# Performance work log

Hardware: AMD Instinct MI355X
Metric: run time of the kernel (lower is better)

## Reference

```python
import jax, jax.numpy as jnp
import numpy as np

NUM_HEADS = 16
D_MODEL = 1024
NUM_LAYERS = 4
VOCAB = 32000
SEQ_LEN = 1024
BATCH = 4
EPS = 1e-6


def position_embedding(seq_len, d_model):
    pos = jnp.arange(seq_len, dtype=jnp.float32)[:, None]
    i = jnp.arange(d_model, dtype=jnp.float32)[None, :]
    # faithful to source: angle_rates = 1 / (1/10000)^(2*(i//2)/d) = 10000^(2*(i//2)/d)
    angle_rates = jnp.power(10000.0, 2.0 * jnp.floor(i / 2.0) / float(d_model))
    ang = pos * angle_rates  # [S, D]
    return jnp.concatenate([jnp.sin(ang[:, 0::2]), jnp.cos(ang[:, 1::2])], axis=-1)[None]  # [1,S,D]


def layer_norm(x, g, b):
    m = jnp.mean(x, axis=-1, keepdims=True)
    v = jnp.mean(jnp.square(x - m), axis=-1, keepdims=True)
    return (x - m) * jax.lax.rsqrt(v + EPS) * g + b


def setup_inputs() -> dict:
    key = jax.random.key(0)
    ks = jax.random.split(key, 20)
    L, D = NUM_LAYERS, D_MODEL
    s = 0.02
    inp = {
        "x": jax.random.randint(ks[0], (BATCH, SEQ_LEN), 0, VOCAB, dtype=jnp.int32),
        "mask": jnp.zeros((BATCH, 1, 1, SEQ_LEN), dtype=jnp.float32),
        "emb": jax.random.normal(ks[1], (VOCAB, D), dtype=jnp.float32) * s,
        "wq": jax.random.normal(ks[2], (L, D, D), dtype=jnp.float32) * s,
        "bq": jnp.zeros((L, D), dtype=jnp.float32),
        "wk": jax.random.normal(ks[3], (L, D, D), dtype=jnp.float32) * s,
        "bk": jnp.zeros((L, D), dtype=jnp.float32),
        "wv": jax.random.normal(ks[4], (L, D, D), dtype=jnp.float32) * s,
        "bv": jnp.zeros((L, D), dtype=jnp.float32),
        "wo": jax.random.normal(ks[5], (L, D, D), dtype=jnp.float32) * s,
        "bo": jnp.zeros((L, D), dtype=jnp.float32),
        "wf": jax.random.normal(ks[6], (L, D, D), dtype=jnp.float32) * s,
        "bf": jnp.zeros((L, D), dtype=jnp.float32),
        "g1": jnp.ones((L, D), dtype=jnp.float32),
        "b1": jnp.zeros((L, D), dtype=jnp.float32),
        "g2": jnp.ones((L, D), dtype=jnp.float32),
        "b2": jnp.zeros((L, D), dtype=jnp.float32),
    }
    return inp


def encoder_forward(x, mask, emb, wq, bq, wk, bk, wv, bv, wo, bo, wf, bf, g1, b1, g2, b2):
    B, S = x.shape
    D = emb.shape[1]
    H = NUM_HEADS
    dh = D // H
    h = emb[x] * jnp.sqrt(jnp.float32(D))  # [B,S,D]
    h = h + position_embedding(S, D)[:, :S, :]

    def split_heads(t):  # [B,S,D] -> [B,H,S,dh]
        return t.reshape(B, S, H, dh).transpose(0, 2, 1, 3)

    for l in range(wq.shape[0]):
        q = split_heads(h @ wq[l] + bq[l])
        k = split_heads(h @ wk[l] + bk[l])
        v = split_heads(h @ wv[l] + bv[l])
        scores = jnp.einsum("bhqd,bhkd->bhqk", q, k) / jnp.sqrt(jnp.float32(dh))
        scores = scores + mask * -1e9
        w = jax.nn.softmax(scores, axis=-1)
        ctx = jnp.einsum("bhqk,bhkd->bhqd", w, v)  # [B,H,S,dh]
        ctx = ctx.transpose(0, 2, 1, 3).reshape(B, S, D)
        attn_out = ctx @ wo[l] + bo[l]
        h = layer_norm(h + attn_out, g1[l], b1[l])
        ff = h @ wf[l] + bf[l]
        h = layer_norm(h + ff, g2[l], b2[l])
    return h


def reference(x, mask, emb, wq, bq, wk, bk, wv, bv, wo, bo, wf, bf, g1, b1, g2, b2):
    return encoder_forward(x, mask, emb, wq, bq, wk, bk, wv, bv, wo, bo, wf, bf, g1, b1, g2, b2)
```

## Files before the change

### kernel.cpp

```cpp
#include <hip/hip_runtime.h>
#include <hip/hip_bf16.h>
#include <math.h>

typedef __hip_bfloat16 bf16;
typedef unsigned int u32;
typedef __attribute__((ext_vector_type(8))) short short8;
typedef __attribute__((ext_vector_type(4))) float f32x4;


#define ATT_LDK 72
#define PS_LD  72

typedef __attribute__((address_space(3))) u32 lds_u32;
typedef const __attribute__((address_space(1))) u32 glb_u32;
static __device__ __forceinline__ void g2l16(const void* g, void* l) {
    __builtin_amdgcn_global_load_lds((glb_u32*)g, (lds_u32*)l, 16, 0, 0);
}

static __device__ __forceinline__ unsigned short bf16bits(float f) {
    bf16 h = __float2bfloat16(f);
    return *(unsigned short*)&h;
}

__global__ __launch_bounds__(256) void wprep_kernel(
    const float* __restrict__ wq, const float* __restrict__ wk,
    const float* __restrict__ wv, const float* __restrict__ wo,
    const float* __restrict__ wf, bf16* __restrict__ wt_all)
{
    __shared__ bf16 tile[64][ATT_LDK];
    const int z = blockIdx.z;
    const int l = z / 5, f = z % 5;
    const float* src = (f == 0) ? wq : (f == 1) ? wk : (f == 2) ? wv : (f == 3) ? wo : wf;
    src += (size_t)l * 1024 * 1024;
    bf16* dst = wt_all + ((size_t)l * 5 + f) * 1024 * 1024;

    const int k0 = blockIdx.x * 64, n0 = blockIdx.y * 64;
    const int t = threadIdx.x;
#pragma unroll
    for (int rr = 0; rr < 4; ++rr) {
        int slot = t + rr * 256;
        int r = slot >> 4, c = slot & 15;
        float4 v = *(const float4*)(src + (size_t)(k0 + r) * 1024 + n0 + c * 4);
        tile[c * 4 + 0][r] = __float2bfloat16(v.x);
        tile[c * 4 + 1][r] = __float2bfloat16(v.y);
        tile[c * 4 + 2][r] = __float2bfloat16(v.z);
        tile[c * 4 + 3][r] = __float2bfloat16(v.w);
    }
    __syncthreads();
#pragma unroll
    for (int rr = 0; rr < 2; ++rr) {
        int slot = t + rr * 256;
        int n = slot >> 3, c = slot & 7;
        *(uint4*)(dst + (size_t)(n0 + n) * 1024 + k0 + c * 8) = *(const uint4*)&tile[n][c * 8];
    }
}

__global__ void bias_stack_kernel(const float* __restrict__ bq, const float* __restrict__ bk,
                                  const float* __restrict__ bv, float* __restrict__ bqkv)
{
    int i = blockIdx.x * 256 + threadIdx.x;
    if (i < 4 * 3072) {
        int l = i / 3072, c = i % 3072;
        int fam = c >> 10, cc = c & 1023;
        const float* s = (fam == 0) ? bq : (fam == 1) ? bk : bv;
        bqkv[i] = s[l * 1024 + cc];
    }
}

__global__ __launch_bounds__(256) void pe_kernel(float* __restrict__ pe)
{
    int idx = blockIdx.x * 256 + threadIdx.x;
    int d0 = (idx & 255) * 4;
    int s = idx >> 8;
    float out[4];
#pragma unroll
    for (int j = 0; j < 4; ++j) {
        int d = d0 + j;
        int m = (d < 512) ? d : (d - 512);
        float ex = (float)(2 * m) * (1.0f / 1024.0f);
        float rate = (float)pow(10000.0, (double)ex);
        float ang = (float)s * rate;
        double a = (double)ang;
        out[j] = (d < 512) ? (float)sin(a) : (float)cos(a);
    }
    *(float4*)(pe + (size_t)s * 1024 + d0) = *(float4*)out;
}

__global__ __launch_bounds__(256) void embed_kernel(
    const int* __restrict__ x, const float* __restrict__ emb,
    const float* __restrict__ pe,
    float* __restrict__ hf, bf16* __restrict__ hb)
{
    int idx = blockIdx.x * 256 + threadIdx.x;
    int d0 = (idx & 255) * 4;
    int row = idx >> 8;
    int s = row & 1023;
    int tok = x[row];
    float4 e = *(const float4*)(emb + (size_t)tok * 1024 + d0);
    float4 p = *(const float4*)(pe + (size_t)s * 1024 + d0);
    float out[4] = {e.x * 32.0f + p.x, e.y * 32.0f + p.y,
                    e.z * 32.0f + p.z, e.w * 32.0f + p.w};
    *(float4*)(hf + (size_t)row * 1024 + d0) = *(float4*)out;
    unsigned short pk[4];
#pragma unroll
    for (int j = 0; j < 4; ++j) pk[j] = bf16bits(out[j]);
    *(uint2*)(hb + (size_t)row * 1024 + d0) = *(uint2*)pk;
}

__global__ __launch_bounds__(256, 3) void gemm_bt_kernel(
    const bf16* __restrict__ A, const bf16* __restrict__ Bt,
    const float* __restrict__ bias,
    bf16* __restrict__ Cb, bf16* __restrict__ VtOut,
    int M, int N, int K)
{
    __shared__ bf16 As[128 * 32];
    __shared__ bf16 Bs[128 * 32];
    __shared__ bf16 Cst[4][16 * PS_LD];
    const int t = threadIdx.x;
    const int lane = t & 63, wave = t >> 6;
    const int wr = wave >> 1, wc = wave & 1;
    const int lidx = lane & 15, quad = lane >> 4;
    const int m0 = blockIdx.x * 128, n0 = blockIdx.y * 128;

    f32x4 acc[4][4];
#pragma unroll
    for (int i = 0; i < 4; ++i)
#pragma unroll
        for (int j = 0; j < 4; ++j) acc[i][j] = (f32x4){0.f, 0.f, 0.f, 0.f};

    const int r0 = wave * 32;
    const int rloc = lane >> 2;
    const int csw = ((lane & 3) ^ ((lane >> 3) & 3)) * 8;
    const bf16* Abase = A  + (size_t)(m0 + r0 + rloc) * K + csw;
    const bf16* Bbase = Bt + (size_t)(n0 + r0 + rloc) * K + csw;
    bf16* AsW = As + r0 * 32;
    bf16* BsW = Bs + r0 * 32;
    const int aslot = (quad ^ ((lidx >> 1) & 3)) * 8;

    for (int k0 = 0; k0 < K; k0 += 32) {
        __syncthreads();
        g2l16(Abase + k0,                  AsW);
        g2l16(Abase + k0 + 16 * (size_t)K, AsW + 16 * 32);
        g2l16(Bbase + k0,                  BsW);
        g2l16(Bbase + k0 + 16 * (size_t)K, BsW + 16 * 32);
        __syncthreads();

        short8 af[4], bfr[4];
#pragma unroll
        for (int i = 0; i < 4; ++i)
            af[i] = *(const short8*)(As + (wr * 64 + i * 16 + lidx) * 32 + aslot);
#pragma unroll
        for (int j = 0; j < 4; ++j)
            bfr[j] = *(const short8*)(Bs + (wc * 64 + j * 16 + lidx) * 32 + aslot);
#pragma unroll
        for (int i = 0; i < 4; ++i)
#pragma unroll
            for (int j = 0; j < 4; ++j)
                acc[i][j] = __builtin_amdgcn_mfma_f32_16x16x32_bf16(af[i], bfr[j], acc[i][j], 0, 0, 0);
    }

    float bvj[4];
#pragma unroll
    for (int j = 0; j < 4; ++j)
        bvj[j] = bias ? bias[n0 + wc * 64 + j * 16 + lidx] : 0.0f;

    if (VtOut && n0 >= 2048) {
        const int bidx = m0 >> 10;
        const int s_base = (m0 & 1023) + wr * 64 + quad * 4;
        const int d_base = (n0 - 2048) + wc * 64;
#pragma unroll
        for (int i = 0; i < 4; ++i)
#pragma unroll
            for (int j = 0; j < 4; ++j) {
                unsigned short pk[4];
#pragma unroll
                for (int r = 0; r < 4; ++r)
                    pk[r] = bf16bits(acc[i][j][r] + bvj[j]);
                bf16* dst = VtOut + ((size_t)bidx * 1024 + d_base + j * 16 + lidx) * 1024
                            + s_base + i * 16;
                *(uint2*)dst = *(const uint2*)pk;
            }
    } else {
        const int row16 = lane >> 2, c4 = lane & 3;
#pragma unroll
        for (int i = 0; i < 4; ++i) {
#pragma unroll
            for (int j = 0; j < 4; ++j)
#pragma unroll
                for (int r = 0; r < 4; ++r)
                    Cst[wave][(quad * 4 + r) * PS_LD + j * 16 + lidx] =
                        __float2bfloat16(acc[i][j][r] + bvj[j]);
            bf16* dst = Cb + (size_t)(m0 + wr * 64 + i * 16 + row16) * N + n0 + wc * 64;
            const bf16* srcr = &Cst[wave][row16 * PS_LD];
#pragma unroll
            for (int h = 0; h < 2; ++h)
                *(uint4*)(dst + (c4 + 4 * h) * 8) = *(const uint4*)(srcr + (c4 + 4 * h) * 8);
        }
    }
}

__global__ __launch_bounds__(256, 4) void gemm64_kernel(
    const bf16* __restrict__ A, const bf16* __restrict__ Bt,
    const float* __restrict__ bias, float* __restrict__ Cf,
    int M, int N, int K)
{
    __shared__ bf16 As[64 * 32];
    __shared__ bf16 Bs[128 * 32];
    const int t = threadIdx.x;
    const int lane = t & 63, wave = t >> 6;
    const int wr = wave >> 1, wc = wave & 1;
    const int lidx = lane & 15, quad = lane >> 4;
    const int m0 = blockIdx.x * 64, n0 = blockIdx.y * 128;

    f32x4 acc[2][4];
#pragma unroll
    for (int i = 0; i < 2; ++i)
#pragma unroll
        for (int j = 0; j < 4; ++j) acc[i][j] = (f32x4){0.f, 0.f, 0.f, 0.f};

    const int rloc = lane >> 2;
    const int csw = ((lane & 3) ^ ((lane >> 3) & 3)) * 8;
    const bf16* Abase = A  + (size_t)(m0 + wave * 16 + rloc) * K + csw;
    const bf16* Bbase = Bt + (size_t)(n0 + wave * 32 + rloc) * K + csw;
    bf16* AsW = As + wave * 16 * 32;
    bf16* BsW = Bs + wave * 32 * 32;
    const int aslot = (quad ^ ((lidx >> 1) & 3)) * 8;

    for (int k0 = 0; k0 < K; k0 += 32) {
        __syncthreads();
        g2l16(Abase + k0,                  AsW);
        g2l16(Bbase + k0,                  BsW);
        g2l16(Bbase + k0 + 16 * (size_t)K, BsW + 16 * 32);
        __syncthreads();

        short8 af[2], bfr[4];
#pragma unroll
        for (int i = 0; i < 2; ++i)
            af[i] = *(const short8*)(As + (wr * 32 + i * 16 + lidx) * 32 + aslot);
#pragma unroll
        for (int j = 0; j < 4; ++j)
            bfr[j] = *(const short8*)(Bs + (wc * 64 + j * 16 + lidx) * 32 + aslot);
#pragma unroll
        for (int i = 0; i < 2; ++i)
#pragma unroll
            for (int j = 0; j < 4; ++j)
                acc[i][j] = __builtin_amdgcn_mfma_f32_16x16x32_bf16(af[i], bfr[j], acc[i][j], 0, 0, 0);
    }

#pragma unroll
    for (int i = 0; i < 2; ++i)
#pragma unroll
        for (int j = 0; j < 4; ++j) {
            int col = n0 + wc * 64 + j * 16 + lidx;
            float bv = bias[col];
#pragma unroll
            for (int r = 0; r < 4; ++r) {
                int rowg = m0 + wr * 32 + i * 16 + quad * 4 + r;
                Cf[(size_t)rowg * N + col] = acc[i][j][r] + bv;
            }
        }
}

__global__ __launch_bounds__(512, 4) void attention_kernel(
    const bf16* __restrict__ QKV,
    const bf16* __restrict__ Vt,
    const float* __restrict__ mask,
    bf16* __restrict__ ctx)
{
    __shared__ bf16 Ks[64 * 64];
    __shared__ bf16 Vs[64 * 64];
    __shared__ bf16 Ps[8][16 * PS_LD];

    const int t = threadIdx.x, lane = t & 63, wave = t >> 6;
    const int quad = lane >> 4, lidx = lane & 15;
    const int b = blockIdx.x >> 4, hh = blockIdx.x & 15;
    const int q0 = blockIdx.y * 128 + wave * 16;

    const int r8 = lane >> 3;
    const int gc = ((lane & 7) ^ r8) * 8;
    const bf16* kg0 = QKV + (size_t)(b * 1024 + wave * 8 + r8) * 3072 + 1024 + hh * 64 + gc;
    const bf16* vg0 = Vt  + (size_t)(b * 1024 + hh * 64 + wave * 8 + r8) * 1024 + gc;
    bf16* KsW = Ks + wave * 8 * 64;
    bf16* VsW = Vs + wave * 8 * 64;

    short8 qf[2];
    {
        const bf16* qp = QKV + (size_t)(b * 1024 + q0 + lidx) * 3072 + hh * 64;
        qf[0] = *(const short8*)(qp + quad * 8);
        qf[1] = *(const short8*)(qp + 32 + quad * 8);
    }

    f32x4 Oacc[4];
#pragma unroll
    for (int nt = 0; nt < 4; ++nt) Oacc[nt] = (f32x4){0.f, 0.f, 0.f, 0.f};
    float psum[4] = {0.f, 0.f, 0.f, 0.f};

    const int fslot = lidx & 7;

    for (int kt = 0; kt < 16; ++kt) {
        __syncthreads();
        g2l16(kg0 + (size_t)kt * 64 * 3072, KsW);
        g2l16(vg0 + kt * 64, VsW);
        __syncthreads();

        f32x4 sacc[4];
#pragma unroll
        for (int nt = 0; nt < 4; ++nt) sacc[nt] = (f32x4){0.f, 0.f, 0.f, 0.f};
#pragma unroll
        for (int kk = 0; kk < 2; ++kk)
#pragma unroll
            for (int nt = 0; nt < 4; ++nt) {
                short8 kf = *(const short8*)(Ks + (nt * 16 + lidx) * 64 + (((kk * 4 + quad) ^ fslot) * 8));
                sacc[nt] = __builtin_amdgcn_mfma_f32_16x16x32_bf16(qf[kk], kf, sacc[nt], 0, 0, 0);
            }

#pragma unroll
        for (int nt = 0; nt < 4; ++nt) {
            float mv = mask[b * 1024 + kt * 64 + nt * 16 + lidx] * -1e9f;
#pragma unroll
            for (int r = 0; r < 4; ++r) {
                float p = __expf(sacc[nt][r] * 0.125f + mv);
                sacc[nt][r] = p;
                psum[r] += p;
            }
        }

#pragma unroll
        for (int nt = 0; nt < 4; ++nt)
#pragma unroll
            for (int r = 0; r < 4; ++r)
                Ps[wave][(quad * 4 + r) * PS_LD + nt * 16 + lidx] = __float2bfloat16(sacc[nt][r]);

#pragma unroll
        for (int kk = 0; kk < 2; ++kk) {
            short8 pf = *(const short8*)(&Ps[wave][lidx * PS_LD + kk * 32 + quad * 8]);
#pragma unroll
            for (int nt = 0; nt < 4; ++nt) {
                short8 vf = *(const short8*)(Vs + (nt * 16 + lidx) * 64 + (((kk * 4 + quad) ^ fslot) * 8));
                Oacc[nt] = __builtin_amdgcn_mfma_f32_16x16x32_bf16(pf, vf, Oacc[nt], 0, 0, 0);
            }
        }
    }

#pragma unroll
    for (int off = 1; off < 16; off <<= 1)
#pragma unroll
        for (int r = 0; r < 4; ++r)
            psum[r] += __shfl_xor(psum[r], off, 64);
    float linv[4];
#pragma unroll
    for (int r = 0; r < 4; ++r) linv[r] = 1.0f / psum[r];

#pragma unroll
    for (int nt = 0; nt < 4; ++nt)
#pragma unroll
        for (int r = 0; r < 4; ++r)
            Ps[wave][(quad * 4 + r) * PS_LD + nt * 16 + lidx] = __float2bfloat16(Oacc[nt][r] * linv[r]);

    const int row16 = lane >> 2, c4 = lane & 3;
    bf16* dst = ctx + (size_t)(b * 1024 + q0 + row16) * 1024 + hh * 64;
    const bf16* srcr = &Ps[wave][row16 * PS_LD];
#pragma unroll
    for (int h = 0; h < 2; ++h)
        *(uint4*)(dst + (c4 + 4 * h) * 8) = *(const uint4*)(srcr + (c4 + 4 * h) * 8);
}

__global__ __launch_bounds__(256) void add_ln_kernel(
    const float* __restrict__ x, const float* __restrict__ dx,
    const float* __restrict__ g, const float* __restrict__ b,
    float* __restrict__ outf, bf16* __restrict__ outb)
{
    __shared__ float red[4];
    const int row = blockIdx.x;
    const int t = threadIdx.x;
    const int c0 = t * 4;
    float4 xv = *(const float4*)(x + (size_t)row * 1024 + c0);
    float4 dv = *(const float4*)(dx + (size_t)row * 1024 + c0);
    float v[4] = {xv.x + dv.x, xv.y + dv.y, xv.z + dv.z, xv.w + dv.w};
    float s = v[0] + v[1] + v[2] + v[3];
#pragma unroll
    for (int off = 1; off < 64; off <<= 1) s += __shfl_xor(s, off, 64);
    if ((t & 63) == 0) red[t >> 6] = s;
    __syncthreads();
    float mean = (red[0] + red[1] + red[2] + red[3]) * (1.0f / 1024.0f);
    float sq = 0.f;
#pragma unroll
    for (int i = 0; i < 4; ++i) { float d = v[i] - mean; sq += d * d; }
#pragma unroll
    for (int off = 1; off < 64; off <<= 1) sq += __shfl_xor(sq, off, 64);
    __syncthreads();
    if ((t & 63) == 0) red[t >> 6] = sq;
    __syncthreads();
    float var = (red[0] + red[1] + red[2] + red[3]) * (1.0f / 1024.0f);
    float rs = rsqrtf(var + 1e-6f);
    float4 gv = *(const float4*)(g + c0);
    float4 bv = *(const float4*)(b + c0);
    float gg[4] = {gv.x, gv.y, gv.z, gv.w}, bb[4] = {bv.x, bv.y, bv.z, bv.w};
    float o[4];
    unsigned short pk[4];
#pragma unroll
    for (int i = 0; i < 4; ++i) {
        o[i] = (v[i] - mean) * rs * gg[i] + bb[i];
        pk[i] = bf16bits(o[i]);
    }
    *(float4*)(outf + (size_t)row * 1024 + c0) = *(float4*)o;
    *(uint2*)(outb + (size_t)row * 1024 + c0) = *(uint2*)pk;
}

extern "C" void kernel_launch(void* const* d_in, const int* in_sizes, int n_in,
                              void* d_out, int out_size, void* d_ws, size_t ws_size,
                              hipStream_t stream)
{
    const int*   x    = (const int*)d_in[0];
    const float* mask = (const float*)d_in[1];
    const float* emb  = (const float*)d_in[2];
    const float* wq   = (const float*)d_in[3];
    const float* bq   = (const float*)d_in[4];
    const float* wk   = (const float*)d_in[5];
    const float* bk   = (const float*)d_in[6];
    const float* wv   = (const float*)d_in[7];
    const float* bv   = (const float*)d_in[8];
    const float* wo   = (const float*)d_in[9];
    const float* bo   = (const float*)d_in[10];
    const float* wf   = (const float*)d_in[11];
    const float* bfp  = (const float*)d_in[12];
    const float* g1   = (const float*)d_in[13];
    const float* b1   = (const float*)d_in[14];
    const float* g2   = (const float*)d_in[15];
    const float* b2   = (const float*)d_in[16];

    char* ws = (char*)d_ws;
    float* h_f  = (float*)ws;                 ws += 4096ull * 1024 * 4;
    bf16*  h_b  = (bf16*)ws;                  ws += 4096ull * 1024 * 2;
    bf16*  qkv  = (bf16*)ws;                  ws += 4096ull * 3072 * 2;
    bf16*  vt   = (bf16*)ws;                  ws += 4096ull * 1024 * 2;
    bf16*  ctx  = (bf16*)ws;                  ws += 4096ull * 1024 * 2;
    bf16*  wt   = (bf16*)ws;                  ws += 20ull * 1024 * 1024 * 2;
    float* pe   = (float*)ws;                 ws += 1024ull * 1024 * 4;
    float* bqkv = (float*)ws;                 ws += 4ull * 3072 * 4;
    float* delta = (float*)qkv;

    wprep_kernel<<<dim3(16, 16, 20), 256, 0, stream>>>(wq, wk, wv, wo, wf, wt);
    bias_stack_kernel<<<dim3(48), 256, 0, stream>>>(bq, bk, bv, bqkv);
    pe_kernel<<<dim3(1024), 256, 0, stream>>>(pe);
    embed_kernel<<<dim3(4096), 256, 0, stream>>>(x, emb, pe, h_f, h_b);

    for (int l = 0; l < 4; ++l) {
        bf16* wt_l = wt + (size_t)l * 5 * 1024 * 1024;
        gemm_bt_kernel<<<dim3(32, 24), 256, 0, stream>>>(
            h_b, wt_l, bqkv + l * 3072, qkv, vt, 4096, 3072, 1024);
        attention_kernel<<<dim3(64, 8), 512, 0, stream>>>(qkv, vt, mask, ctx);
        gemm64_kernel<<<dim3(64, 8), 256, 0, stream>>>(
            ctx, wt_l + 3ull * 1024 * 1024, bo + l * 1024, delta, 4096, 1024, 1024);
        add_ln_kernel<<<dim3(4096), 256, 0, stream>>>(
            h_f, delta, g1 + l * 1024, b1 + l * 1024, h_f, h_b);
        gemm64_kernel<<<dim3(64, 8), 256, 0, stream>>>(
            h_b, wt_l + 4ull * 1024 * 1024, bfp + l * 1024, delta, 4096, 1024, 1024);
        float* outf = (l == 3) ? (float*)d_out : h_f;
        add_ln_kernel<<<dim3(4096), 256, 0, stream>>>(
            h_f, delta, g2 + l * 1024, b2 + l * 1024, outf, h_b);
    }
    (void)in_sizes; (void)n_in; (void)out_size; (void)ws_size;
}
```

Before: 782.2 us.

## Split-K 128x128 GEMM for out/FF projections and smaller attention blocks

Replaces the 64x128 output/FFN GEMM with a 128x128 tile kernel that splits K in two, writing two fp32 partial buffers that the add+LayerNorm kernel sums. This raises per-block data reuse while keeping the block count at 512. Attention is also changed from 512-thread blocks covering 128 queries to 256-thread blocks covering 64 queries, doubling the grid, with each wave loading twice as many K/V rows. The trade-off is an extra 16MB fp32 partial write and read per GEMM, plus more redundant K/V loading in attention.

```diff
diff --git a/kernel.cpp b/kernel.cpp
--- a/kernel.cpp
+++ b/kernel.cpp
@@ -199,69 +199,74 @@
     }
 }
 
-__global__ __launch_bounds__(256, 4) void gemm64_kernel(
+__global__ __launch_bounds__(256, 2) void gemm_sk_kernel(
     const bf16* __restrict__ A, const bf16* __restrict__ Bt,
     const float* __restrict__ bias, float* __restrict__ Cf,
     int M, int N, int K)
 {
-    __shared__ bf16 As[64 * 32];
+    __shared__ bf16 As[128 * 32];
     __shared__ bf16 Bs[128 * 32];
     const int t = threadIdx.x;
     const int lane = t & 63, wave = t >> 6;
     const int wr = wave >> 1, wc = wave & 1;
     const int lidx = lane & 15, quad = lane >> 4;
-    const int m0 = blockIdx.x * 64, n0 = blockIdx.y * 128;
-
-    f32x4 acc[2][4];
-#pragma unroll
-    for (int i = 0; i < 2; ++i)
+    const int m0 = blockIdx.x * 128, n0 = blockIdx.y * 128;
+    const int kz = blockIdx.z;
+    const int kbeg = kz * (K >> 1), kend = kbeg + (K >> 1);
+
+    f32x4 acc[4][4];
+#pragma unroll
+    for (int i = 0; i < 4; ++i)
 #pragma unroll
         for (int j = 0; j < 4; ++j) acc[i][j] = (f32x4){0.f, 0.f, 0.f, 0.f};
 
+    const int r0 = wave * 32;
     const int rloc = lane >> 2;
     const int csw = ((lane & 3) ^ ((lane >> 3) & 3)) * 8;
-    const bf16* Abase = A  + (size_t)(m0 + wave * 16 + rloc) * K + csw;
-    const bf16* Bbase = Bt + (size_t)(n0 + wave * 32 + rloc) * K + csw;
-    bf16* AsW = As + wave * 16 * 32;
-    bf16* BsW = Bs + wave * 32 * 32;
+    const bf16* Abase = A  + (size_t)(m0 + r0 + rloc) * K + csw;
+    const bf16* Bbase = Bt + (size_t)(n0 + r0 + rloc) * K + csw;
+    bf16* AsW = As + r0 * 32;
+    bf16* BsW = Bs + r0 * 32;
     const int aslot = (quad ^ ((lidx >> 1) & 3)) * 8;
 
-    for (int k0 = 0; k0 < K; k0 += 32) {
+    for (int k0 = kbeg; k0 < kend; k0 += 32) {
         __syncthreads();
         g2l16(Abase + k0,                  AsW);
+        g2l16(Abase + k0 + 16 * (size_t)K, AsW + 16 * 32);
         g2l16(Bbase + k0,                  BsW);
         g2l16(Bbase + k0 + 16 * (size_t)K, BsW + 16 * 32);
         __syncthreads();
 
-        short8 af[2], bfr[4];
-#pragma unroll
-        for (int i = 0; i < 2; ++i)
-            af[i] = *(const short8*)(As + (wr * 32 + i * 16 + lidx) * 32 + aslot);
+        short8 af[4], bfr[4];
+#pragma unroll
+        for (int i = 0; i < 4; ++i)
+            af[i] = *(const short8*)(As + (wr * 64 + i * 16 + lidx) * 32 + aslot);
 #pragma unroll
         for (int j = 0; j < 4; ++j)
             bfr[j] = *(const short8*)(Bs + (wc * 64 + j * 16 + lidx) * 32 + aslot);
 #pragma unroll
-        for (int i = 0; i < 2; ++i)
+        for (int i = 0; i < 4; ++i)
 #pragma unroll
             for (int j = 0; j < 4; ++j)
                 acc[i][j] = __builtin_amdgcn_mfma_f32_16x16x32_bf16(af[i], bfr[j], acc[i][j], 0, 0, 0);
     }
 
-#pragma unroll
-    for (int i = 0; i < 2; ++i)
+    float* out = Cf + (size_t)kz * M * N;
+#pragma unroll
+    for (int i = 0; i < 4; ++i)
 #pragma unroll
         for (int j = 0; j < 4; ++j) {
             int col = n0 + wc * 64 + j * 16 + lidx;
-            float bv = bias[col];
+            float bv = (kz == 0) ? bias[col] : 0.0f;
 #pragma unroll
             for (int r = 0; r < 4; ++r) {
-                int rowg = m0 + wr * 32 + i * 16 + quad * 4 + r;
-                Cf[(size_t)rowg * N + col] = acc[i][j][r] + bv;
+                int rowg = m0 + wr * 64 + i * 16 + quad * 4 + r;
+                out[(size_t)rowg * N + col] = acc[i][j][r] + bv;
             }
         }
 }
 
-__global__ __launch_bounds__(512, 4) void attention_kernel(
+__global__ __launch_bounds__(256, 4) void attention_kernel(
     const bf16* __restrict__ QKV,
     const bf16* __restrict__ Vt,
     const float* __restrict__ mask,
@@ -269,19 +274,19 @@
 {
     __shared__ bf16 Ks[64 * 64];
     __shared__ bf16 Vs[64 * 64];
-    __shared__ bf16 Ps[8][16 * PS_LD];
+    __shared__ bf16 Ps[4][16 * PS_LD];
 
     const int t = threadIdx.x, lane = t & 63, wave = t >> 6;
     const int quad = lane >> 4, lidx = lane & 15;
     const int b = blockIdx.x >> 4, hh = blockIdx.x & 15;
-    const int q0 = blockIdx.y * 128 + wave * 16;
+    const int q0 = blockIdx.y * 64 + wave * 16;
 
     const int r8 = lane >> 3;
     const int gc = ((lane & 7) ^ r8) * 8;
-    const bf16* kg0 = QKV + (size_t)(b * 1024 + wave * 8 + r8) * 3072 + 1024 + hh * 64 + gc;
-    const bf16* vg0 = Vt  + (size_t)(b * 1024 + hh * 64 + wave * 8 + r8) * 1024 + gc;
-    bf16* KsW = Ks + wave * 8 * 64;
-    bf16* VsW = Vs + wave * 8 * 64;
+    const bf16* kg0 = QKV + (size_t)(b * 1024 + wave * 16 + r8) * 3072 + 1024 + hh * 64 + gc;
+    const bf16* vg0 = Vt  + (size_t)(b * 1024 + hh * 64 + wave * 16 + r8) * 1024 + gc;
+    bf16* KsW = Ks + wave * 16 * 64;
+    bf16* VsW = Vs + wave * 16 * 64;
 
     short8 qf[2];
     {
@@ -299,8 +304,10 @@
 
     for (int kt = 0; kt < 16; ++kt) {
         __syncthreads();
-        g2l16(kg0 + (size_t)kt * 64 * 3072, KsW);
-        g2l16(vg0 + kt * 64, VsW);
+        g2l16(kg0 + (size_t)kt * 64 * 3072,       KsW);
+        g2l16(kg0 + (size_t)(kt * 64 + 8) * 3072, KsW + 8 * 64);
+        g2l16(vg0 + kt * 64,                      VsW);
+        g2l16(vg0 + 8 * 1024 + kt * 64,           VsW + 8 * 64);
         __syncthreads();
 
         f32x4 sacc[4];
@@ -366,7 +373,8 @@
 }
 
 __global__ __launch_bounds__(256) void add_ln_kernel(
-    const float* __restrict__ x, const float* __restrict__ dx,
+    const float* __restrict__ x, const float* __restrict__ dx0,
+    const float* __restrict__ dx1,
     const float* __restrict__ g, const float* __restrict__ b,
     float* __restrict__ outf, bf16* __restrict__ outb)
 {
@@ -375,8 +383,10 @@
     const int t = threadIdx.x;
     const int c0 = t * 4;
     float4 xv = *(const float4*)(x + (size_t)row * 1024 + c0);
-    float4 dv = *(const float4*)(dx + (size_t)row * 1024 + c0);
-    float v[4] = {xv.x + dv.x, xv.y + dv.y, xv.z + dv.z, xv.w + dv.w};
+    float4 d0 = *(const float4*)(dx0 + (size_t)row * 1024 + c0);
+    float4 d1 = *(const float4*)(dx1 + (size_t)row * 1024 + c0);
+    float v[4] = {xv.x + d0.x + d1.x, xv.y + d0.y + d1.y,
+                  xv.z + d0.z + d1.z, xv.w + d0.w + d1.w};
     float s = v[0] + v[1] + v[2] + v[3];
 #pragma unroll
     for (int off = 1; off < 64; off <<= 1) s += __shfl_xor(s, off, 64);
@@ -430,15 +440,16 @@
     const float* b2   = (const float*)d_in[16];
 
     char* ws = (char*)d_ws;
-    float* h_f  = (float*)ws;                 ws += 4096ull * 1024 * 4;
-    bf16*  h_b  = (bf16*)ws;                  ws += 4096ull * 1024 * 2;
-    bf16*  qkv  = (bf16*)ws;                  ws += 4096ull * 3072 * 2;
-    bf16*  vt   = (bf16*)ws;                  ws += 4096ull * 1024 * 2;
-    bf16*  ctx  = (bf16*)ws;                  ws += 4096ull * 1024 * 2;
-    bf16*  wt   = (bf16*)ws;                  ws += 20ull * 1024 * 1024 * 2;
-    float* pe   = (float*)ws;                 ws += 1024ull * 1024 * 4;
-    float* bqkv = (float*)ws;                 ws += 4ull * 3072 * 4;
-    float* delta = (float*)qkv;
+    float* h_f   = (float*)ws;                ws += 4096ull * 1024 * 4;
+    bf16*  h_b   = (bf16*)ws;                 ws += 4096ull * 1024 * 2;
+    bf16*  qkv   = (bf16*)ws;                 ws += 4096ull * 3072 * 2;
+    bf16*  vt    = (bf16*)ws;                 ws += 4096ull * 1024 * 2;
+    bf16*  ctx   = (bf16*)ws;                 ws += 4096ull * 1024 * 2;
+    bf16*  wt    = (bf16*)ws;                 ws += 20ull * 1024 * 1024 * 2;
+    float* pe    = (float*)ws;                ws += 1024ull * 1024 * 4;
+    float* delta = (float*)ws;                ws += 2ull * 4096 * 1024 * 4;
+    float* bqkv  = (float*)ws;                ws += 4ull * 3072 * 4;
+    float* delta1 = delta + 4096ull * 1024;
 
     wprep_kernel<<<dim3(16, 16, 20), 256, 0, stream>>>(wq, wk, wv, wo, wf, wt);
     bias_stack_kernel<<<dim3(48), 256, 0, stream>>>(bq, bk, bv, bqkv);
@@ -449,16 +460,16 @@
         bf16* wt_l = wt + (size_t)l * 5 * 1024 * 1024;
         gemm_bt_kernel<<<dim3(32, 24), 256, 0, stream>>>(
             h_b, wt_l, bqkv + l * 3072, qkv, vt, 4096, 3072, 1024);
-        attention_kernel<<<dim3(64, 8), 512, 0, stream>>>(qkv, vt, mask, ctx);
-        gemm64_kernel<<<dim3(64, 8), 256, 0, stream>>>(
+        attention_kernel<<<dim3(64, 16), 256, 0, stream>>>(qkv, vt, mask, ctx);
+        gemm_sk_kernel<<<dim3(32, 8, 2), 256, 0, stream>>>(
             ctx, wt_l + 3ull * 1024 * 1024, bo + l * 1024, delta, 4096, 1024, 1024);
         add_ln_kernel<<<dim3(4096), 256, 0, stream>>>(
-            h_f, delta, g1 + l * 1024, b1 + l * 1024, h_f, h_b);
-        gemm64_kernel<<<dim3(64, 8), 256, 0, stream>>>(
+            h_f, delta, delta1, g1 + l * 1024, b1 + l * 1024, h_f, h_b);
+        gemm_sk_kernel<<<dim3(32, 8, 2), 256, 0, stream>>>(
             h_b, wt_l + 4ull * 1024 * 1024, bfp + l * 1024, delta, 4096, 1024, 1024);
         float* outf = (l == 3) ? (float*)d_out : h_f;
         add_ln_kernel<<<dim3(4096), 256, 0, stream>>>(
-            h_f, delta, g2 + l * 1024, b2 + l * 1024, outf, h_b);
+            h_f, delta, delta1, g2 + l * 1024, b2 + l * 1024, outf, h_b);
     }
     (void)in_sizes; (void)n_in; (void)out_size; (void)ws_size;
 }
```

Result: no change. 784.3 us (+0.3%).
